# Optimization experiments

Hardware: AMD Instinct MI355X
Metric: run time of the kernel (lower is better)

Reference implementation:

```python
import jax, jax.numpy as jnp
import numpy as np

DIM = 256
NUM_HEADS = 4
HEAD_DIM = DIM // NUM_HEADS
EPS = 1e-5


def setup_inputs() -> dict:
    key = jax.random.key(0)
    ks = jax.random.split(key, 8)
    B, N, C = 8, 2048, DIM
    s = 0.02
    return {
        "x": jax.random.normal(ks[0], (B, N, C), jnp.float32),
        "qkv_w": jax.random.normal(ks[1], (C, 3 * C), jnp.float32) * s,
        "qkv_b": jnp.zeros((3 * C,), jnp.float32),
        "proj_w": jax.random.normal(ks[2], (C, C), jnp.float32) * s,
        "proj_b": jnp.zeros((C,), jnp.float32),
        "ln1_g": jnp.ones((C,), jnp.float32),
        "ln1_b": jnp.zeros((C,), jnp.float32),
        "ln2_g": jnp.ones((C,), jnp.float32),
        "ln2_b": jnp.zeros((C,), jnp.float32),
        "mlp_w1": jax.random.normal(ks[3], (C, 2 * C), jnp.float32) * s,
        "mlp_b1": jnp.zeros((2 * C,), jnp.float32),
        "mlp_w2": jax.random.normal(ks[4], (2 * C, C), jnp.float32) * s,
        "mlp_b2": jnp.zeros((C,), jnp.float32),
    }


def _layernorm(x, g, b):
    mu = jnp.mean(x, axis=-1, keepdims=True)
    var = jnp.mean(jnp.square(x - mu), axis=-1, keepdims=True)
    return (x - mu) * jax.lax.rsqrt(var + EPS) * g + b


def reference(x, qkv_w, qkv_b, proj_w, proj_b, ln1_g, ln1_b, ln2_g, ln2_b,
              mlp_w1, mlp_b1, mlp_w2, mlp_b2):
    B, N, C = x.shape
    H, D = NUM_HEADS, HEAD_DIM
    shortcut = x
    h = _layernorm(x, ln1_g, ln1_b)
    qkv = (h @ qkv_w + qkv_b).reshape(B, N, 3, H, D)
    q = qkv[:, :, 0].transpose(0, 2, 1, 3)  # [B,H,N,D]
    k = qkv[:, :, 1].transpose(0, 2, 1, 3)
    v = qkv[:, :, 2].transpose(0, 2, 1, 3)
    attn = jnp.einsum('bhnd,bhmd->bhnm', q, k) * (D ** -0.5)
    attn = jax.nn.softmax(attn, axis=-1)  # dropout = identity (eval mode)
    o = jnp.einsum('bhnm,bhmd->bhnd', attn, v)
    o = o.transpose(0, 2, 1, 3).reshape(B, N, C)
    x = o @ proj_w + proj_b + shortcut
    h2 = _layernorm(x, ln2_g, ln2_b)
    mlp = jax.nn.gelu(h2 @ mlp_w1 + mlp_b1, approximate=False) @ mlp_w2 + mlp_b2
    return x + mlp
```

## Files before the change

kernel.cpp:

```cpp
#include <hip/hip_runtime.h>

typedef __bf16 bf16;
typedef __bf16 bf16x8 __attribute__((ext_vector_type(8)));
typedef __bf16 bf16x4 __attribute__((ext_vector_type(4)));
typedef float  f32x4  __attribute__((ext_vector_type(4)));
typedef unsigned u32x2 __attribute__((ext_vector_type(2)));

typedef __attribute__((address_space(1))) const void GASV;
typedef __attribute__((address_space(3))) void LASV;

__device__ __forceinline__ void gload16(const void* g, void* l) {
  __builtin_amdgcn_global_load_lds((GASV*)g, (LASV*)l, 16, 0, 0);
}

constexpr float CEXP = 0.125f * 1.44269504088896340736f;

__global__ __launch_bounds__(256) void wconv_all(const float* __restrict__ qkv_w,
                                                 const float* __restrict__ proj_w,
                                                 const float* __restrict__ w1,
                                                 const float* __restrict__ w2,
                                                 bf16* __restrict__ Wtqkv,
                                                 bf16* __restrict__ WtP,
                                                 bf16* __restrict__ Wt1,
                                                 bf16* __restrict__ Wt2) {
  __shared__ float td[32][33];
  const int t = blockIdx.x;
  const float* src;
  bf16* dst;
  int Kin, Nin, kt, nt;
  if (t < 192)      { src = qkv_w; dst = Wtqkv; Kin = 256; Nin = 768; kt = t & 7;          nt = t >> 3; }
  else if (t < 256) { src = proj_w; dst = WtP;  Kin = 256; Nin = 256; kt = (t - 192) & 7;  nt = (t - 192) >> 3; }
  else if (t < 384) { src = w1;    dst = Wt1;   Kin = 256; Nin = 512; kt = (t - 256) & 7;  nt = (t - 256) >> 3; }
  else              { src = w2;    dst = Wt2;   Kin = 512; Nin = 256; kt = (t - 384) & 15; nt = (t - 384) >> 4; }
  const int tid = threadIdx.x;
  {
    const int r = tid >> 3, c4 = (tid & 7) << 2;
    const float4 v = *(const float4*)(src + (size_t)(kt * 32 + r) * Nin + nt * 32 + c4);
    td[r][c4 + 0] = v.x; td[r][c4 + 1] = v.y; td[r][c4 + 2] = v.z; td[r][c4 + 3] = v.w;
  }
  __syncthreads();
  {
    const int n = tid >> 3, k4 = (tid & 7) << 2;
    bf16x4 o;
#pragma unroll
    for (int i = 0; i < 4; ++i) o[i] = (bf16)td[k4 + i][n];
    *(bf16x4*)(dst + (size_t)(nt * 32 + n) * Kin + kt * 32 + k4) = o;
  }
}

__global__ __launch_bounds__(256) void ln_fwd(const float* __restrict__ x,
                                              const float* __restrict__ gam,
                                              const float* __restrict__ bet,
                                              bf16* __restrict__ out) {
  const int lane = threadIdx.x & 63;
  const int w = threadIdx.x >> 6;
  const size_t row = (size_t)blockIdx.x * 4 + w;
  const float4 v = *(const float4*)(x + row * 256 + lane * 4);
  float s1 = v.x + v.y + v.z + v.w;
  float s2 = v.x * v.x + v.y * v.y + v.z * v.z + v.w * v.w;
#pragma unroll
  for (int m = 1; m < 64; m <<= 1) {
    s1 += __shfl_xor(s1, m);
    s2 += __shfl_xor(s2, m);
  }
  const float mu = s1 * (1.0f / 256.0f);
  const float var = s2 * (1.0f / 256.0f) - mu * mu;
  const float rs = rsqrtf(var + 1e-5f);
  const float4 g4 = *(const float4*)(gam + lane * 4);
  const float4 b4 = *(const float4*)(bet + lane * 4);
  bf16x4 o;
  o[0] = (bf16)((v.x - mu) * rs * g4.x + b4.x);
  o[1] = (bf16)((v.y - mu) * rs * g4.y + b4.y);
  o[2] = (bf16)((v.z - mu) * rs * g4.z + b4.z);
  o[3] = (bf16)((v.w - mu) * rs * g4.w + b4.w);
  *(bf16x4*)(out + row * 256 + lane * 4) = o;
}

template <int EPI>
__global__ __launch_bounds__(256) void gemm_bt(const bf16* __restrict__ A,
                                               const bf16* __restrict__ Bt,
                                               const float* __restrict__ bias,
                                               const float* __restrict__ res,
                                               void* __restrict__ outp,
                                               int M, int N, int K,
                                               const bf16* __restrict__ A2,
                                               const float* __restrict__ pstats) {
  constexpr bool MA = (EPI == 4);
  __shared__ bf16 Al[2][8192];
  __shared__ bf16 Bl[2][8192];
  const int tid = threadIdx.x;
  const int lane = tid & 63;
  const int W = tid >> 6;
  const int wm = W >> 1, wn = W & 1;
  const int qi = lane & 15, g = lane >> 4;
  const int nbm = M >> 7;
  const int bm = (int)blockIdx.x % nbm;
  const int bn = (int)blockIdx.x / nbm;
  const int m0 = bm << 7, n0 = bn << 7;
  const int nk = K >> 6;

  int rowg[4];
  const char* asrc[4];
  const char* bsrc[4];
#pragma unroll
  for (int p = 0; p < 4; ++p) {
    const int s = W * 4 + p;
    const int row = (s >> 3) * 64 + ((s >> 1) & 3) * 16 + qi;
    const int kb = (s & 1) * 64 + g * 16;
    rowg[p] = m0 + row;
    asrc[p] = (const char*)(A + (size_t)(m0 + row) * K) + kb;
    bsrc[p] = (const char*)(Bt + (size_t)(n0 + row) * K) + kb;
  }

  f32x4 acc[4][4];
#pragma unroll
  for (int i = 0; i < 4; ++i)
#pragma unroll
    for (int j = 0; j < 4; ++j) acc[i][j] = (f32x4){0.f, 0.f, 0.f, 0.f};

  bf16x8 pa0v[4], pa1v[4];
  float2 sst0[4], sst1[4];

  auto stagePlain = [&](int sl) {
#pragma unroll
    for (int p = 0; p < 4; ++p) {
      gload16(asrc[p], (char*)&Al[sl][0] + (W * 4 + p) * 1024);
      gload16(bsrc[p], (char*)&Bl[sl][0] + (W * 4 + p) * 1024);
      asrc[p] += 128;
      bsrc[p] += 128;
    }
  };
  auto stageMAload = [&](int sl, int t) {
#pragma unroll
    for (int p = 0; p < 4; ++p) {
      gload16(bsrc[p], (char*)&Bl[sl][0] + (W * 4 + p) * 1024);
      bsrc[p] += 128;
      pa0v[p] = *(const bf16x8*)(asrc[p]);
      pa1v[p] = *(const bf16x8*)((const char*)A2 + (asrc[p] - (const char*)A));
      asrc[p] += 128;
      const int bh = ((rowg[p] >> 11) << 2) + t;
      const int ql = rowg[p] & 2047;
      sst0[p] = *(const float2*)(pstats + ((size_t)bh * 2048 + ql) * 2);
      sst1[p] = *(const float2*)(pstats + ((size_t)(bh + 32) * 2048 + ql) * 2);
    }
  };
  auto stageMAwrite = [&](int sl) {
#pragma unroll
    for (int p = 0; p < 4; ++p) {
      const float mx = fmaxf(sst0[p].x, sst1[p].x);
      float a0 = exp2f(CEXP * (sst0[p].x - mx));
      float a1 = exp2f(CEXP * (sst1[p].x - mx));
      const float inv = 1.0f / (sst0[p].y * a0 + sst1[p].y * a1);
      a0 *= inv;
      a1 *= inv;
      bf16x8 wv;
#pragma unroll
      for (int j = 0; j < 8; ++j)
        wv[j] = (bf16)((float)pa0v[p][j] * a0 + (float)pa1v[p][j] * a1);
      *(bf16x8*)((char*)&Al[sl][0] + (W * 4 + p) * 1024 + lane * 16) = wv;
    }
  };

  if constexpr (MA) {
    stageMAload(0, 0);
    stageMAwrite(0);
  } else {
    stagePlain(0);
  }
  asm volatile("s_waitcnt vmcnt(0)" ::: "memory");
  if constexpr (MA) asm volatile("s_waitcnt lgkmcnt(0)" ::: "memory");
  __builtin_amdgcn_s_barrier();

  for (int t = 0; t < nk; ++t) {
    if (t + 1 < nk) {
      if constexpr (MA) stageMAload((t + 1) & 1, t + 1);
      else stagePlain((t + 1) & 1);
    }
    const char* pa = (const char*)&Al[t & 1][0] + wm * 8192 + lane * 16;
    const char* pb = (const char*)&Bl[t & 1][0] + wn * 8192 + lane * 16;
    bf16x8 av[4][2], bv[4][2];
#pragma unroll
    for (int f = 0; f < 4; ++f)
#pragma unroll
      for (int ks = 0; ks < 2; ++ks) {
        av[f][ks] = *(const bf16x8*)(pa + (f * 2 + ks) * 1024);
        bv[f][ks] = *(const bf16x8*)(pb + (f * 2 + ks) * 1024);
      }
    __builtin_amdgcn_s_setprio(1);
#pragma unroll
    for (int fm = 0; fm < 4; ++fm)
#pragma unroll
      for (int fn = 0; fn < 4; ++fn) {
        acc[fm][fn] = __builtin_amdgcn_mfma_f32_16x16x32_bf16(av[fm][0], bv[fn][0], acc[fm][fn], 0, 0, 0);
        acc[fm][fn] = __builtin_amdgcn_mfma_f32_16x16x32_bf16(av[fm][1], bv[fn][1], acc[fm][fn], 0, 0, 0);
      }
    __builtin_amdgcn_s_setprio(0);
    if (t + 1 < nk) {
      if constexpr (MA) stageMAwrite((t + 1) & 1);
    }
    asm volatile("s_waitcnt vmcnt(0)" ::: "memory");
    if constexpr (MA) asm volatile("s_waitcnt lgkmcnt(0)" ::: "memory");
    __builtin_amdgcn_s_barrier();
  }

#pragma unroll
  for (int fm = 0; fm < 4; ++fm)
#pragma unroll
    for (int fn = 0; fn < 4; ++fn) {
      const int r0 = m0 + wm * 64 + fm * 16 + ((lane >> 4) << 2);
      const int c = n0 + wn * 64 + fn * 16 + (lane & 15);
#pragma unroll
      for (int j = 0; j < 4; ++j) {
        const int r = r0 + j;
        const float v = acc[fm][fn][j];
        if constexpr (EPI == 0) {
          ((bf16*)outp)[(size_t)r * N + c] = (bf16)(v + bias[c]);
        } else if constexpr (EPI == 1) {
          ((bf16*)outp)[(size_t)r * 2048 + ((size_t)(c >> 11)) * 524288 + (c & 2047)] =
              (bf16)(v + bias[r]);
        } else if constexpr (EPI == 2 || EPI == 4) {
          ((float*)outp)[(size_t)r * N + c] = v + bias[c] + res[(size_t)r * N + c];
        } else {
          const float u = v + bias[c];
          ((bf16*)outp)[(size_t)r * N + c] = (bf16)(u * 0.5f * (1.0f + erff(u * 0.70710678118f)));
        }
      }
    }
}

__global__ __launch_bounds__(256) void attn_fwd(const bf16* __restrict__ qk,
                                                const bf16* __restrict__ vT,
                                                bf16* __restrict__ po0,
                                                bf16* __restrict__ po1,
                                                float* __restrict__ pstats) {
  __shared__ bf16 Kl[2][4096];
  __shared__ bf16 Vl[2][4096];
  __shared__ bf16 Pl[4][1024];
  const int tid = threadIdx.x;
  const int lane = tid & 63;
  const int w = tid >> 6;
  const int g = lane >> 4;
  const int qi = lane & 15;
  const int bid = (int)blockIdx.x;
  const int bh = bid & 31;
  const int qt = (bid >> 5) & 15;
  const int s = bid >> 9;
  const int b = bh >> 2, h = bh & 3;

  const size_t qrow0 = (size_t)b * 2048 + qt * 128 + w * 32 + qi;
  bf16x8 qf[2][2];
#pragma unroll
  for (int f = 0; f < 2; ++f) {
    const bf16* qp = qk + (qrow0 + f * 16) * 512 + h * 64 + g * 8;
    qf[f][0] = *(const bf16x8*)qp;
    qf[f][1] = *(const bf16x8*)(qp + 32);
  }

  float mrun[2] = {0.f, 0.f};
  float lsum[2] = {0.f, 0.f};
  f32x4 o[4][2];
#pragma unroll
  for (int i = 0; i < 4; ++i)
#pragma unroll
    for (int f = 0; f < 2; ++f) o[i][f] = (f32x4){0.f, 0.f, 0.f, 0.f};

  constexpr float THR = 8.0f / CEXP;

  const char* kbase = (const char*)qk + ((size_t)b * 2048) * 1024 + 512 + h * 128 +
                      (size_t)s * 16 * 65536;
  const char* vbase = (const char*)vT + (size_t)bh * 262144 + (size_t)s * 16 * 128;
  const char* ks[2];
  const char* vs[2];
#pragma unroll
  for (int i = 0; i < 2; ++i) {
    const int fk = i * 2 + (w >> 1);
    const int half = w & 1;
    ks[i] = kbase + (fk * 16 + qi) * 1024 + half * 64 + g * 16;
    vs[i] = vbase + (size_t)(fk * 16 + qi) * 4096 + half * 64 + g * 16;
  }
  char* const pw = (char*)&Pl[w][0];
  int paddrb[2];
#pragma unroll
  for (int bb = 0; bb < 2; ++bb)
    paddrb[bb] = (bb * 2 + (g >> 1)) * 256 + qi * 16 + (g & 1) * 8;
  const char* const prd = pw + lane * 16;

  auto stage = [&](int slot) {
    char* kd = (char*)&Kl[0][0] + slot * 8192 + w * 1024;
    char* vd = (char*)&Vl[0][0] + slot * 8192 + w * 1024;
    gload16(ks[0], kd);
    gload16(ks[1], kd + 4096);
    gload16(vs[0], vd);
    gload16(vs[1], vd + 4096);
    ks[0] += 65536; ks[1] += 65536;
    vs[0] += 128;   vs[1] += 128;
  };

  stage(0);
  asm volatile("s_waitcnt vmcnt(0)" ::: "memory");
  __builtin_amdgcn_s_barrier();

  for (int t = 0; t < 16; ++t) {
    if (t < 15) stage((t + 1) & 1);
    const char* kb = (const char*)&Kl[0][0] + (t & 1) * 8192 + lane * 16;
    f32x4 st[4][2];
    __builtin_amdgcn_s_setprio(1);
#pragma unroll
    for (int fk = 0; fk < 4; ++fk) {
      const bf16x8 k0 = *(const bf16x8*)(kb + fk * 2048);
      const bf16x8 k1 = *(const bf16x8*)(kb + fk * 2048 + 1024);
#pragma unroll
      for (int f = 0; f < 2; ++f) {
        f32x4 z = (f32x4){0.f, 0.f, 0.f, 0.f};
        st[fk][f] = __builtin_amdgcn_mfma_f32_16x16x32_bf16(k0, qf[f][0], z, 0, 0, 0);
        st[fk][f] = __builtin_amdgcn_mfma_f32_16x16x32_bf16(k1, qf[f][1], st[fk][f], 0, 0, 0);
      }
    }
    __builtin_amdgcn_s_setprio(0);
    float pmax[2];
#pragma unroll
    for (int f = 0; f < 2; ++f) {
      float m0 = fmaxf(fmaxf(st[0][f][0], st[0][f][1]), fmaxf(st[0][f][2], st[0][f][3]));
      float m1 = fmaxf(fmaxf(st[1][f][0], st[1][f][1]), fmaxf(st[1][f][2], st[1][f][3]));
      float m2 = fmaxf(fmaxf(st[2][f][0], st[2][f][1]), fmaxf(st[2][f][2], st[2][f][3]));
      float m3 = fmaxf(fmaxf(st[3][f][0], st[3][f][1]), fmaxf(st[3][f][2], st[3][f][3]));
      pmax[f] = fmaxf(fmaxf(m0, m1), fmaxf(m2, m3));
    }
    if (!__all(pmax[0] <= mrun[0] + THR && pmax[1] <= mrun[1] + THR)) {
#pragma unroll
      for (int f = 0; f < 2; ++f) {
        float mt = fmaxf(pmax[f], __shfl_xor(pmax[f], 16));
        mt = fmaxf(mt, __shfl_xor(mt, 32));
        const float mnew = fmaxf(mrun[f], mt);
        const float alpha = exp2f(CEXP * (mrun[f] - mnew));
        lsum[f] *= alpha;
#pragma unroll
        for (int fd = 0; fd < 4; ++fd)
#pragma unroll
          for (int j = 0; j < 4; ++j) o[fd][f][j] *= alpha;
        mrun[f] = mnew;
      }
    }
    unsigned pk[4][2][2];
#pragma unroll
    for (int f = 0; f < 2; ++f) {
      const float negcm = -CEXP * mrun[f];
      float ts = 0.f;
#pragma unroll
      for (int fk = 0; fk < 4; ++fk)
#pragma unroll
        for (int jp = 0; jp < 2; ++jp) {
          const float p0 = exp2f(fmaf(st[fk][f][2 * jp], CEXP, negcm));
          const float p1 = exp2f(fmaf(st[fk][f][2 * jp + 1], CEXP, negcm));
          ts += p0 + p1;
          union { bf16 h2[2]; unsigned u; } cv;
          cv.h2[0] = (bf16)p0;
          cv.h2[1] = (bf16)p1;
          pk[fk][f][jp] = cv.u;
        }
      lsum[f] += ts;
    }
    const char* vb = (const char*)&Vl[0][0] + (t & 1) * 8192 + lane * 16;
#pragma unroll
    for (int ksl = 0; ksl < 2; ++ksl) {
#pragma unroll
      for (int bb = 0; bb < 2; ++bb) {
        const int fk = 2 * ksl + bb;
#pragma unroll
        for (int f = 0; f < 2; ++f) {
          u32x2 pv2;
          pv2[0] = pk[fk][f][0];
          pv2[1] = pk[fk][f][1];
          *(u32x2*)(pw + f * 1024 + paddrb[bb]) = pv2;
        }
      }
      bf16x8 pa[2];
#pragma unroll
      for (int f = 0; f < 2; ++f) pa[f] = *(const bf16x8*)(prd + f * 1024);
      __builtin_amdgcn_s_setprio(1);
#pragma unroll
      for (int fd = 0; fd < 4; ++fd) {
        const bf16x8 vv = *(const bf16x8*)(vb + fd * 2048 + ksl * 1024);
#pragma unroll
        for (int f = 0; f < 2; ++f)
          o[fd][f] = __builtin_amdgcn_mfma_f32_16x16x32_bf16(vv, pa[f], o[fd][f], 0, 0, 0);
      }
      __builtin_amdgcn_s_setprio(0);
    }
    asm volatile("s_waitcnt vmcnt(0)" ::: "memory");
    __builtin_amdgcn_s_barrier();
  }

#pragma unroll
  for (int f = 0; f < 2; ++f) {
    float l = lsum[f];
    l += __shfl_xor(l, 16);
    l += __shfl_xor(l, 32);
    lsum[f] = l;
  }
  if (g == 0) {
#pragma unroll
    for (int f = 0; f < 2; ++f) {
      float2 sv;
      sv.x = mrun[f];
      sv.y = lsum[f];
      *(float2*)(pstats + (((size_t)s * 32 + bh) * 2048 + qt * 128 + w * 32 + f * 16 + qi) * 2) = sv;
    }
  }
  bf16* const pob = s ? po1 : po0;
#pragma unroll
  for (int f = 0; f < 2; ++f) {
    bf16* const orow = pob + (qrow0 + f * 16) * 256 + h * 64 + g * 4;
#pragma unroll
    for (int fd = 0; fd < 4; ++fd) {
      bf16x4 ov;
#pragma unroll
      for (int j = 0; j < 4; ++j) ov[j] = (bf16)o[fd][f][j];
      *(bf16x4*)(orow + fd * 16) = ov;
    }
  }
}

extern "C" void kernel_launch(void* const* d_in, const int* in_sizes, int n_in,
                              void* d_out, int out_size, void* d_ws, size_t ws_size,
                              hipStream_t stream) {
  const float* x      = (const float*)d_in[0];
  const float* qkv_w  = (const float*)d_in[1];
  const float* qkv_b  = (const float*)d_in[2];
  const float* proj_w = (const float*)d_in[3];
  const float* proj_b = (const float*)d_in[4];
  const float* ln1_g  = (const float*)d_in[5];
  const float* ln1_b  = (const float*)d_in[6];
  const float* ln2_g  = (const float*)d_in[7];
  const float* ln2_b  = (const float*)d_in[8];
  const float* mlp_w1 = (const float*)d_in[9];
  const float* mlp_b1 = (const float*)d_in[10];
  const float* mlp_w2 = (const float*)d_in[11];
  const float* mlp_b2 = (const float*)d_in[12];
  float* out = (float*)d_out;

  char* ws = (char*)d_ws;
  bf16* Wtqkv = (bf16*)(ws);
  bf16* WtP   = (bf16*)(ws + 393216);
  bf16* Wt1   = (bf16*)(ws + 524288);
  bf16* Wt2   = (bf16*)(ws + 786432);
  bf16* h     = (bf16*)(ws + 1048576);
  bf16* qkb   = (bf16*)(ws + 9437184);
  bf16* vT    = (bf16*)(ws + 26214400);
  bf16* po1   = (bf16*)(ws + 34603008);
  float* x2   = (float*)(ws + 42991616);
  float* pstats = (float*)(ws + 59768832);
  bf16* po0 = h;
  bf16* a1 = qkb;
  bf16* h2 = h;

  wconv_all<<<512, 256, 0, stream>>>(qkv_w, proj_w, mlp_w1, mlp_w2, Wtqkv, WtP, Wt1, Wt2);

  ln_fwd<<<4096, 256, 0, stream>>>(x, ln1_g, ln1_b, h);
  gemm_bt<0><<<512, 256, 0, stream>>>(h, Wtqkv, qkv_b, nullptr, qkb, 16384, 512, 256, nullptr, nullptr);
  gemm_bt<1><<<256, 256, 0, stream>>>(Wtqkv + 512 * 256, h, qkv_b + 512, nullptr, vT, 256, 16384, 256, nullptr, nullptr);
  attn_fwd<<<1024, 256, 0, stream>>>(qkb, vT, po0, po1, pstats);
  gemm_bt<4><<<256, 256, 0, stream>>>(po0, WtP, proj_b, x, x2, 16384, 256, 256, po1, pstats);
  ln_fwd<<<4096, 256, 0, stream>>>(x2, ln2_g, ln2_b, h2);
  gemm_bt<3><<<512, 256, 0, stream>>>(h2, Wt1, mlp_b1, nullptr, a1, 16384, 512, 256, nullptr, nullptr);
  gemm_bt<2><<<256, 256, 0, stream>>>(a1, Wt2, mlp_b2, x2, out, 16384, 256, 512, nullptr, nullptr);
}
```

Measured before the change: 178.2 us.

## Load K/V tiles directly into registers with double-buffered prefetch instead of LDS

Replaces the shared-memory staging of K and V tiles (global_load_lds plus a barrier each iteration) with direct global-to-register loads into two register buffers, ping-ponged across an unrolled pair of iterations. Each wave now loads all 64 keys/values itself instead of sharing LDS tiles across the four waves. This removes the LDS round trip and block-wide barriers but quadruples global/L2 traffic for K/V and adds many VGPRs, which may reduce occupancy.

```diff
diff --git a/kernel.cpp b/kernel.cpp
--- a/kernel.cpp
+++ b/kernel.cpp
@@ -233,8 +233,6 @@
                                                 bf16* __restrict__ po0,
                                                 bf16* __restrict__ po1,
                                                 float* __restrict__ pstats) {
-  __shared__ bf16 Kl[2][4096];
-  __shared__ bf16 Vl[2][4096];
   __shared__ bf16 Pl[4][1024];
   const int tid = threadIdx.x;
   const int lane = tid & 63;
@@ -269,15 +267,14 @@
   const char* kbase = (const char*)qk + ((size_t)b * 2048) * 1024 + 512 + h * 128 +
                       (size_t)s * 16 * 65536;
   const char* vbase = (const char*)vT + (size_t)bh * 262144 + (size_t)s * 16 * 128;
-  const char* ks[2];
-  const char* vs[2];
-#pragma unroll
-  for (int i = 0; i < 2; ++i) {
-    const int fk = i * 2 + (w >> 1);
-    const int half = w & 1;
-    ks[i] = kbase + (fk * 16 + qi) * 1024 + half * 64 + g * 16;
-    vs[i] = vbase + (size_t)(fk * 16 + qi) * 4096 + half * 64 + g * 16;
-  }
+  const char* kp[4];
+  const char* vp[4];
+#pragma unroll
+  for (int fk = 0; fk < 4; ++fk) {
+    kp[fk] = kbase + (fk * 16 + qi) * 1024 + g * 16;
+    vp[fk] = vbase + (size_t)(fk * 16 + qi) * 4096 + g * 16;
+  }
+
   char* const pw = (char*)&Pl[w][0];
   int paddrb[2];
 #pragma unroll
@@ -285,37 +282,31 @@
     paddrb[bb] = (bb * 2 + (g >> 1)) * 256 + qi * 16 + (g & 1) * 8;
   const char* const prd = pw + lane * 16;
 
-  auto stage = [&](int slot) {
-    char* kd = (char*)&Kl[0][0] + slot * 8192 + w * 1024;
-    char* vd = (char*)&Vl[0][0] + slot * 8192 + w * 1024;
-    gload16(ks[0], kd);
-    gload16(ks[1], kd + 4096);
-    gload16(vs[0], vd);
-    gload16(vs[1], vd + 4096);
-    ks[0] += 65536; ks[1] += 65536;
-    vs[0] += 128;   vs[1] += 128;
+  bf16x8 kA[4][2], vA[4][2], kB[4][2], vB[4][2];
+
+  auto LOAD = [&](bf16x8 (&kr)[4][2], bf16x8 (&vr)[4][2]) {
+#pragma unroll
+    for (int fk = 0; fk < 4; ++fk) {
+      kr[fk][0] = *(const bf16x8*)(kp[fk]);
+      kr[fk][1] = *(const bf16x8*)(kp[fk] + 64);
+      vr[fk][0] = *(const bf16x8*)(vp[fk]);
+      vr[fk][1] = *(const bf16x8*)(vp[fk] + 64);
+      kp[fk] += 65536;
+      vp[fk] += 128;
+    }
   };
 
-  stage(0);
-  asm volatile("s_waitcnt vmcnt(0)" ::: "memory");
-  __builtin_amdgcn_s_barrier();
-
-  for (int t = 0; t < 16; ++t) {
-    if (t < 15) stage((t + 1) & 1);
-    const char* kb = (const char*)&Kl[0][0] + (t & 1) * 8192 + lane * 16;
+  auto COMPUTE = [&](bf16x8 (&kr)[4][2], bf16x8 (&vr)[4][2]) {
     f32x4 st[4][2];
     __builtin_amdgcn_s_setprio(1);
 #pragma unroll
-    for (int fk = 0; fk < 4; ++fk) {
-      const bf16x8 k0 = *(const bf16x8*)(kb + fk * 2048);
-      const bf16x8 k1 = *(const bf16x8*)(kb + fk * 2048 + 1024);
+    for (int fk = 0; fk < 4; ++fk)
 #pragma unroll
       for (int f = 0; f < 2; ++f) {
         f32x4 z = (f32x4){0.f, 0.f, 0.f, 0.f};
-        st[fk][f] = __builtin_amdgcn_mfma_f32_16x16x32_bf16(k0, qf[f][0], z, 0, 0, 0);
-        st[fk][f] = __builtin_amdgcn_mfma_f32_16x16x32_bf16(k1, qf[f][1], st[fk][f], 0, 0, 0);
-      }
-    }
+        st[fk][f] = __builtin_amdgcn_mfma_f32_16x16x32_bf16(kr[fk][0], qf[f][0], z, 0, 0, 0);
+        st[fk][f] = __builtin_amdgcn_mfma_f32_16x16x32_bf16(kr[fk][1], qf[f][1], st[fk][f], 0, 0, 0);
+      }
     __builtin_amdgcn_s_setprio(0);
     float pmax[2];
 #pragma unroll
@@ -360,7 +351,6 @@
         }
       lsum[f] += ts;
     }
-    const char* vb = (const char*)&Vl[0][0] + (t & 1) * 8192 + lane * 16;
 #pragma unroll
     for (int ksl = 0; ksl < 2; ++ksl) {
 #pragma unroll
@@ -379,16 +369,21 @@
       for (int f = 0; f < 2; ++f) pa[f] = *(const bf16x8*)(prd + f * 1024);
       __builtin_amdgcn_s_setprio(1);
 #pragma unroll
-      for (int fd = 0; fd < 4; ++fd) {
-        const bf16x8 vv = *(const bf16x8*)(vb + fd * 2048 + ksl * 1024);
+      for (int fd = 0; fd < 4; ++fd)
 #pragma unroll
         for (int f = 0; f < 2; ++f)
-          o[fd][f] = __builtin_amdgcn_mfma_f32_16x16x32_bf16(vv, pa[f], o[fd][f], 0, 0, 0);
-      }
+          o[fd][f] = __builtin_amdgcn_mfma_f32_16x16x32_bf16(vr[fd][ksl], pa[f], o[fd][f], 0, 0, 0);
       __builtin_amdgcn_s_setprio(0);
     }
-    asm volatile("s_waitcnt vmcnt(0)" ::: "memory");
-    __builtin_amdgcn_s_barrier();
+  };
+
+  LOAD(kA, vA);
+#pragma unroll 1
+  for (int tt = 0; tt < 8; ++tt) {
+    LOAD(kB, vB);
+    COMPUTE(kA, vA);
+    if (tt < 7) LOAD(kA, vA);
+    COMPUTE(kB, vB);
   }
 
 #pragma unroll
```

Result: slower. 224.7 us (+26.1%).
